# Optimization experiments

Hardware: AMD Instinct MI355X
Metric: run time of the kernel (lower is better)

Reference implementation:

```python
import jax, jax.numpy as jnp
import numpy as np

STATIC_SEQ_DIM = 48  # STAT_DIM(27) + X_TIME_DIM(13) + 8
HIDDEN = 128


def setup_inputs() -> dict:
    key = jax.random.key(0)
    ks = jax.random.split(key, 8)
    B, T = 4096, 512

    def n(k, shape, scale):
        return jax.random.normal(k, shape, dtype=jnp.float32) * scale

    return {
        "y_flow": jax.random.normal(ks[0], (B, T, 1), dtype=jnp.float32),
        "x_statics": jax.random.normal(ks[1], (B, T, STATIC_SEQ_DIM), dtype=jnp.float32),
        "twin_idx": 256,
        "enc_w1": n(ks[2], (STATIC_SEQ_DIM, STATIC_SEQ_DIM), 0.1),
        "enc_b1": jnp.zeros((STATIC_SEQ_DIM,), jnp.float32),
        "enc_w2": n(ks[3], (STATIC_SEQ_DIM, STATIC_SEQ_DIM), 0.1),
        "enc_b2": jnp.zeros((STATIC_SEQ_DIM,), jnp.float32),
        "w_ih": n(ks[4], (4 * HIDDEN, 1 + STATIC_SEQ_DIM), 0.05),
        "w_hh": n(ks[5], (4 * HIDDEN, HIDDEN), 0.05),
        "b_ih": jnp.zeros((4 * HIDDEN,), jnp.float32),
        "b_hh": jnp.zeros((4 * HIDDEN,), jnp.float32),
        "out_w": n(ks[6], (1, HIDDEN), 0.05),
        "out_b": jnp.zeros((1,), jnp.float32),
    }


def reference(y_flow, x_statics, enc_w1, enc_b1, enc_w2, enc_b2,
              w_ih, w_hh, b_ih, b_hh, out_w, out_b, twin_idx):
    B, T, _ = y_flow.shape
    H = w_hh.shape[1]
    # Static encoder MLP has no cross-time dependency -> vectorize over (B, T-1)
    xs = x_statics[:, : T - 1]                                        # (B,T-1,S)
    enc = jax.nn.relu(xs @ enc_w1.T + enc_b1) @ enc_w2.T + enc_b2     # (B,T-1,S)
    enc_t = jnp.swapaxes(enc, 0, 1)                                   # (T-1,B,S)
    flow_t = jnp.swapaxes(y_flow[:, : T - 1], 0, 1)                   # (T-1,B,1)
    ts = jnp.arange(T - 1)

    def step(carry, x):
        h, c, last_pred = carry
        flow_teacher, e_t, t = x
        flow = jnp.where(t < twin_idx - 1, flow_teacher, last_pred)   # (B,1)
        x_in = jnp.concatenate([flow, e_t], axis=-1)                  # (B,1+S)
        gates = x_in @ w_ih.T + b_ih + h @ w_hh.T + b_hh              # (B,4H)
        i, f, g, o = jnp.split(gates, 4, axis=-1)                     # torch gate order
        c_new = jax.nn.sigmoid(f) * c + jax.nn.sigmoid(i) * jnp.tanh(g)
        h_new = jax.nn.sigmoid(o) * jnp.tanh(c_new)
        pred = h_new @ out_w.T + out_b                                # (B,1)
        return (h_new, c_new, pred), pred

    h0 = jnp.zeros((B, H), jnp.float32)
    c0 = jnp.zeros((B, H), jnp.float32)
    p0 = jnp.zeros((B, 1), jnp.float32)
    _, preds = jax.lax.scan(step, (h0, c0, p0), (flow_t, enc_t, ts))  # (T-1,B,1)
    return jnp.swapaxes(preds, 0, 1)                                  # (B,T-1,1)
```

## Files before the change

### kernel.cpp

```cpp
#include <hip/hip_runtime.h>
#include <hip/hip_bf16.h>

#define HID 128
#define SDIM 48
#define NSTEP 511
#define TFULL 512
#define ROWS 16
#define XHS 200
#define HSTR 136
#define O1S 88
#define WENC_OFF 98304
#define BIAS_BYTE_OFF 208896
#define ENC_BYTE_OFF 211200
#define ENC_BYTES (4096ULL*TFULL*SDIM*2ULL)

typedef unsigned short u16;
typedef unsigned int   u32;
typedef __attribute__((ext_vector_type(8))) short short8;
typedef __attribute__((ext_vector_type(4))) float f32x4;

__device__ __forceinline__ float frcp(float x)  { return __builtin_amdgcn_rcpf(x); }
__device__ __forceinline__ float sigm(float x)  { return frcp(1.0f + __expf(-x)); }
__device__ __forceinline__ float tanh_f(float x){ return 1.0f - 2.0f*frcp(1.0f + __expf(2.0f*x)); }
__device__ __forceinline__ u16 f2bf(float f) {
  __hip_bfloat16 h = __float2bfloat16(f);
  return *reinterpret_cast<u16*>(&h);
}
__device__ __forceinline__ u32 pk2(float a, float b) {
  return (u32)f2bf(a) | ((u32)f2bf(b) << 16);
}
__device__ __forceinline__ short8 pack8(float4 a, float4 b) {
  short8 r;
  r[0]=(short)f2bf(a.x); r[1]=(short)f2bf(a.y); r[2]=(short)f2bf(a.z); r[3]=(short)f2bf(a.w);
  r[4]=(short)f2bf(b.x); r[5]=(short)f2bf(b.y); r[6]=(short)f2bf(b.z); r[7]=(short)f2bf(b.w);
  return r;
}

__global__ void setup_weights(const float* __restrict__ w_ih, const float* __restrict__ w_hh,
                              const float* __restrict__ b_ih, const float* __restrict__ b_hh,
                              const float* __restrict__ enc_w1, const float* __restrict__ enc_w2,
                              u16* __restrict__ frags, float* __restrict__ bias, int hfirst) {
  int stride = gridDim.x * blockDim.x;
  int i0 = blockIdx.x * blockDim.x + threadIdx.x;
  for (int idx = i0; idx < 32*6*64*8; idx += stride) {
    int j  = idx & 7;
    int l  = (idx >> 3) & 63;
    int kt = (idx >> 9) % 6;
    int mt = (idx >> 9) / 6;
    int gr = mt*16 + (l & 15);
    int k  = kt*32 + (l >> 4)*8 + j;
    float v = 0.f;
    if (hfirst) {
      if (k < HID)       v = w_hh[gr*HID + k];
      else if (k < 176)  v = w_ih[gr*49 + 1 + (k - HID)];
    } else {
      if (k < 48)        v = w_ih[gr*49 + 1 + k];
      else if (k < 176)  v = w_hh[gr*HID + (k - 48)];
    }
    frags[idx] = f2bf(v);
  }
  for (int idx = i0; idx < 2*3*2*64*8; idx += stride) {
    int j   = idx & 7;
    int l   = (idx >> 3) & 63;
    int kt  = (idx >> 9) & 1;
    int mt  = (idx >> 10) % 3;
    int lyr = (idx >> 10) / 3;
    int row = mt*16 + (l & 15);
    int k   = kt*32 + (l >> 4)*8 + j;
    float v = 0.f;
    if (k < SDIM) v = (lyr ? enc_w2 : enc_w1)[row*SDIM + k];
    frags[WENC_OFF + idx] = f2bf(v);
  }
  for (int idx = i0; idx < 512; idx += stride)
    bias[idx] = b_ih[idx] + b_hh[idx];
}

__global__ __launch_bounds__(256)
void enc_pre(const float* __restrict__ x_statics,
             const float* __restrict__ enc_b1, const float* __restrict__ enc_b2,
             const u16* __restrict__ frags, u16* __restrict__ enc_buf) {
  __shared__ __attribute__((aligned(16))) u16 s_o1[4][ROWS][O1S];
  const int tid = threadIdx.x;
  const int w  = tid >> 6;
  const int l  = tid & 63;
  const int lr = l & 15;
  const int lg = l >> 4;
  const int b     = blockIdx.x >> 3;
  const int chunk = blockIdx.x & 7;
  const int t = chunk*64 + w*16 + lr;

  short8 we1[3][2], we2[3][2];
  f32x4 a[3], e[3];
  #pragma unroll
  for (int mt = 0; mt < 3; ++mt) {
    #pragma unroll
    for (int kt = 0; kt < 2; ++kt) {
      we1[mt][kt] = *(const short8*)(frags + WENC_OFF + (((0*3 + mt)*2 + kt)*64 + l)*8);
      we2[mt][kt] = *(const short8*)(frags + WENC_OFF + (((1*3 + mt)*2 + kt)*64 + l)*8);
    }
    a[mt] = *(const f32x4*)&enc_b1[mt*16 + lg*4];
    e[mt] = *(const f32x4*)&enc_b2[mt*16 + lg*4];
  }

  *(unsigned long long*)&s_o1[w][l & 15][48 + (l >> 4)*4] = 0ULL;

  const float* xbase = x_statics + ((size_t)b*TFULL + t)*SDIM;
  float4 zf4 = make_float4(0.f,0.f,0.f,0.f);
  float4 c0a = *(const float4*)(xbase + lg*8);
  float4 c0b = *(const float4*)(xbase + lg*8 + 4);
  float4 c1a = zf4, c1b = zf4;
  if (lg < 2) {
    c1a = *(const float4*)(xbase + 32 + lg*8);
    c1b = *(const float4*)(xbase + 32 + lg*8 + 4);
  }
  short8 bx0 = pack8(c0a, c0b);
  short8 bx1 = pack8(c1a, c1b);

  #pragma unroll
  for (int mt = 0; mt < 3; ++mt) {
    a[mt] = __builtin_amdgcn_mfma_f32_16x16x32_bf16(we1[mt][0], bx0, a[mt], 0, 0, 0);
    a[mt] = __builtin_amdgcn_mfma_f32_16x16x32_bf16(we1[mt][1], bx1, a[mt], 0, 0, 0);
  }
  #pragma unroll
  for (int mt = 0; mt < 3; ++mt) {
    u32 lo = pk2(fmaxf(a[mt][0],0.f), fmaxf(a[mt][1],0.f));
    u32 hi = pk2(fmaxf(a[mt][2],0.f), fmaxf(a[mt][3],0.f));
    *(uint2*)&s_o1[w][lr][mt*16 + lg*4] = make_uint2(lo, hi);
  }
  asm volatile("s_waitcnt lgkmcnt(0)" ::: "memory");
  __builtin_amdgcn_sched_barrier(0);
  short8 bo0 = *(const short8*)&s_o1[w][lr][lg*8];
  short8 bo1 = *(const short8*)&s_o1[w][lr][32 + lg*8];
  #pragma unroll
  for (int mt = 0; mt < 3; ++mt) {
    e[mt] = __builtin_amdgcn_mfma_f32_16x16x32_bf16(we2[mt][0], bo0, e[mt], 0, 0, 0);
    e[mt] = __builtin_amdgcn_mfma_f32_16x16x32_bf16(we2[mt][1], bo1, e[mt], 0, 0, 0);
  }
  if (t < NSTEP) {
    u16* dst = enc_buf + ((size_t)b*TFULL + t)*SDIM;
    #pragma unroll
    for (int mt = 0; mt < 3; ++mt)
      *(uint2*)(dst + mt*16 + lg*4) = make_uint2(pk2(e[mt][0], e[mt][1]), pk2(e[mt][2], e[mt][3]));
  }
}

__global__ __launch_bounds__(512, 2)
void lstm_pre(const float* __restrict__ y_flow,
              const int* __restrict__ twin_p,
              const float* __restrict__ out_w, const float* __restrict__ out_b,
              const float* __restrict__ w_ih,
              const u16* __restrict__ frags, const float* __restrict__ bias,
              const u16* __restrict__ enc_buf,
              float* __restrict__ out) {
  __shared__ __attribute__((aligned(16))) u16   s_h[2][ROWS][HSTR];
  __shared__ __attribute__((aligned(16))) float s_pp[2][8][ROWS];

  const int tid = threadIdx.x;
  const int blk = blockIdx.x;
  const int w  = tid >> 6;
  const int l  = tid & 63;
  const int lr = l & 15;
  const int lg = l >> 4;
  const size_t b0 = (size_t)blk * ROWS;

  short8 wf[4][6];
  #pragma unroll
  for (int q = 0; q < 4; ++q)
    #pragma unroll
    for (int kt = 0; kt < 6; ++kt)
      wf[q][kt] = *(const short8*)(frags + (((w + 8*q)*6 + kt)*64 + l)*8);

  float wfl[4][4];
  #pragma unroll
  for (int q = 0; q < 4; ++q)
    #pragma unroll
    for (int r = 0; r < 4; ++r)
      wfl[q][r] = w_ih[((w + 8*q)*16 + lg*4 + r)*49];

  f32x4 bgv[4];
  #pragma unroll
  for (int q = 0; q < 4; ++q)
    bgv[q] = *(const f32x4*)&bias[(w + 8*q)*16 + lg*4];

  float owv[4];
  #pragma unroll
  for (int r = 0; r < 4; ++r) owv[r] = out_w[w*16 + lg*4 + r];
  const float ob  = out_b[0];
  const int   twc = twin_p[0] - 1;

  const u16*   erow = enc_buf + (size_t)(b0 + lr)*TFULL*SDIM;
  const float* yrow = y_flow  + (size_t)(b0 + lr)*TFULL;

  short8 encA = *(const short8*)(erow + lg*8);
  short8 encB = {};
  if (lg < 2) encB = *(const short8*)(erow + 32 + lg*8);

  for (int i = tid; i < 2*ROWS*HSTR; i += 512) ((u16*)s_h)[i] = 0;
  for (int i = tid; i < 2*8*ROWS;   i += 512) ((float*)s_pp)[i] = 0.f;
  float c_reg[4] = {0.f, 0.f, 0.f, 0.f};
  __syncthreads();

  for (int st = 0; st < NSTEP; ++st) {
    const int p  = st & 1;
    const int p2 = p ^ 1;

    short8 bh[6];
    #pragma unroll
    for (int kt = 0; kt < 4; ++kt)
      bh[kt] = *(const short8*)&s_h[p][lr][kt*32 + lg*8];
    bh[4] = encA;
    bh[5] = encB;

    float tf = 0.f;
    if (st < twc) tf = yrow[st];

    const int tt = (st + 1 < NSTEP) ? (st + 1) : (NSTEP - 1);
    encA = *(const short8*)(erow + (size_t)tt*SDIM + lg*8);
    encB = (short8){};
    if (lg < 2) encB = *(const short8*)(erow + (size_t)tt*SDIM + 32 + lg*8);

    f32x4 acc[4];
    #pragma unroll
    for (int q = 0; q < 4; ++q) acc[q] = bgv[q];
    #pragma unroll
    for (int kt = 0; kt < 6; ++kt)
      #pragma unroll
      for (int q = 0; q < 4; ++q)
        acc[q] = __builtin_amdgcn_mfma_f32_16x16x32_bf16(wf[q][kt], bh[kt], acc[q], 0, 0, 0);

    float pp01 = s_pp[p][0][lr] + s_pp[p][1][lr];
    float pp23 = s_pp[p][2][lr] + s_pp[p][3][lr];
    float pp45 = s_pp[p][4][lr] + s_pp[p][5][lr];
    float pp67 = s_pp[p][6][lr] + s_pp[p][7][lr];
    float pred_prev = ((pp01 + pp23) + (pp45 + pp67)) + ob;
    if (st == 0) pred_prev = 0.f;
    if (st > 0 && l < 16 && (l >> 1) == w)
      out[(b0 + l)*NSTEP + (st - 1)] = pred_prev;

    const float flow = (st < twc) ? tf : pred_prev;

    float hv[4];
    float hsum = 0.f;
    #pragma unroll
    for (int r = 0; r < 4; ++r) {
      float g_i = acc[0][r] + wfl[0][r]*flow;
      float g_f = acc[1][r] + wfl[1][r]*flow;
      float g_g = acc[2][r] + wfl[2][r]*flow;
      float g_o = acc[3][r] + wfl[3][r]*flow;
      float iv = sigm(g_i);
      float fv = sigm(g_f);
      float gv = tanh_f(g_g);
      float ov = sigm(g_o);
      float c  = fv*c_reg[r] + iv*gv;
      c_reg[r] = c;
      hv[r] = ov*tanh_f(c);
      hsum += hv[r]*owv[r];
    }
    *(uint2*)&s_h[p2][lr][w*16 + lg*4] = make_uint2(pk2(hv[0], hv[1]), pk2(hv[2], hv[3]));
    hsum += __shfl_xor(hsum, 16);
    hsum += __shfl_xor(hsum, 32);
    if (l < 16) s_pp[p2][w][l] = hsum;
    __syncthreads();
  }

  const int pe = NSTEP & 1;
  float pp01 = s_pp[pe][0][lr] + s_pp[pe][1][lr];
  float pp23 = s_pp[pe][2][lr] + s_pp[pe][3][lr];
  float pp45 = s_pp[pe][4][lr] + s_pp[pe][5][lr];
  float pp67 = s_pp[pe][6][lr] + s_pp[pe][7][lr];
  if (l < 16 && (l >> 1) == w)
    out[(b0 + l)*NSTEP + (NSTEP - 1)] = ((pp01 + pp23) + (pp45 + pp67)) + ob;
}

__global__ __launch_bounds__(512, 2)
void lstm_fb(const float* __restrict__ y_flow,
             const float* __restrict__ x_statics,
             const int* __restrict__ twin_p,
             const float* __restrict__ enc_b1, const float* __restrict__ enc_b2,
             const float* __restrict__ out_w, const float* __restrict__ out_b,
             const float* __restrict__ w_ih,
             const u16* __restrict__ frags, const float* __restrict__ bias,
             float* __restrict__ out) {
  __shared__ __attribute__((aligned(16))) u16   s_xh[2][ROWS][XHS];
  __shared__ __attribute__((aligned(16))) u16   s_o1[ROWS][O1S];
  __shared__ __attribute__((aligned(16))) float s_pp[2][ROWS][8];
  __shared__ __attribute__((aligned(16))) float s_bias[512];
  __shared__ __attribute__((aligned(16))) float s_eb1[SDIM];
  __shared__ __attribute__((aligned(16))) float s_eb2[SDIM];

  const int tid = threadIdx.x;
  const int blk = blockIdx.x;
  const int w  = tid >> 6;
  const int l  = tid & 63;
  const int lr = l & 15;
  const int lg = l >> 4;
  const size_t b0 = (size_t)blk * ROWS;

  short8 wf[4][6];
  #pragma unroll
  for (int q = 0; q < 4; ++q)
    #pragma unroll
    for (int kt = 0; kt < 6; ++kt)
      wf[q][kt] = *(const short8*)(frags + (((w + 8*q)*6 + kt)*64 + l)*8);

  float wfl[4][4];
  #pragma unroll
  for (int q = 0; q < 4; ++q)
    #pragma unroll
    for (int r = 0; r < 4; ++r)
      wfl[q][r] = w_ih[((w + 8*q)*16 + lg*4 + r)*49];

  short8 we1[3][2], we2[3][2];
  if (w == 7) {
    #pragma unroll
    for (int mt = 0; mt < 3; ++mt)
      #pragma unroll
      for (int kt = 0; kt < 2; ++kt) {
        we1[mt][kt] = *(const short8*)(frags + WENC_OFF + (((0*3 + mt)*2 + kt)*64 + l)*8);
        we2[mt][kt] = *(const short8*)(frags + WENC_OFF + (((1*3 + mt)*2 + kt)*64 + l)*8);
      }
  }

  float owv[4];
  #pragma unroll
  for (int r = 0; r < 4; ++r) owv[r] = out_w[w*16 + lg*4 + r];
  const float ob  = out_b[0];
  const int   twc = twin_p[0] - 1;

  for (int i = tid; i < 2*ROWS*XHS; i += 512) ((u16*)s_xh)[i] = 0;
  for (int i = tid; i < ROWS*O1S;  i += 512) ((u16*)s_o1)[i] = 0;
  for (int i = tid; i < 2*ROWS*8;  i += 512) ((float*)s_pp)[i] = 0.f;
  s_bias[tid] = bias[tid];
  if (tid < SDIM) { s_eb1[tid] = enc_b1[tid]; s_eb2[tid] = enc_b2[tid]; }
  __syncthreads();

  const float* xrow = x_statics + (size_t)(b0 + lr)*TFULL*SDIM;
  const float* yrow = y_flow    + (size_t)(b0 + lr)*TFULL;

  auto enc_step = [&](short8 bx0, short8 bx1, int pp) {
    f32x4 a[3];
    #pragma unroll
    for (int mt = 0; mt < 3; ++mt) a[mt] = *(const f32x4*)&s_eb1[mt*16 + lg*4];
    #pragma unroll
    for (int mt = 0; mt < 3; ++mt) {
      a[mt] = __builtin_amdgcn_mfma_f32_16x16x32_bf16(we1[mt][0], bx0, a[mt], 0, 0, 0);
      a[mt] = __builtin_amdgcn_mfma_f32_16x16x32_bf16(we1[mt][1], bx1, a[mt], 0, 0, 0);
    }
    #pragma unroll
    for (int mt = 0; mt < 3; ++mt) {
      *(u32*)&s_o1[lr][mt*16 + lg*4]     = pk2(fmaxf(a[mt][0],0.f), fmaxf(a[mt][1],0.f));
      *(u32*)&s_o1[lr][mt*16 + lg*4 + 2] = pk2(fmaxf(a[mt][2],0.f), fmaxf(a[mt][3],0.f));
    }
    asm volatile("s_waitcnt lgkmcnt(0)" ::: "memory");
    __builtin_amdgcn_sched_barrier(0);
    short8 bo0 = *(const short8*)&s_o1[lr][lg*8];
    short8 bo1 = *(const short8*)&s_o1[lr][32 + lg*8];
    f32x4 e[3];
    #pragma unroll
    for (int mt = 0; mt < 3; ++mt) e[mt] = *(const f32x4*)&s_eb2[mt*16 + lg*4];
    #pragma unroll
    for (int mt = 0; mt < 3; ++mt) {
      e[mt] = __builtin_amdgcn_mfma_f32_16x16x32_bf16(we2[mt][0], bo0, e[mt], 0, 0, 0);
      e[mt] = __builtin_amdgcn_mfma_f32_16x16x32_bf16(we2[mt][1], bo1, e[mt], 0, 0, 0);
    }
    #pragma unroll
    for (int mt = 0; mt < 3; ++mt) {
      *(u32*)&s_xh[pp][lr][mt*16 + lg*4]     = pk2(e[mt][0], e[mt][1]);
      *(u32*)&s_xh[pp][lr][mt*16 + lg*4 + 2] = pk2(e[mt][2], e[mt][3]);
    }
  };
  auto load_xs = [&](int t, float4& a0, float4& b0_, float4& a1, float4& b1_) {
    a0 = *(const float4*)(xrow + (size_t)t*SDIM + lg*8);
    b0_= *(const float4*)(xrow + (size_t)t*SDIM + lg*8 + 4);
    if (lg < 2) {
      a1 = *(const float4*)(xrow + (size_t)t*SDIM + 32 + lg*8);
      b1_= *(const float4*)(xrow + (size_t)t*SDIM + 32 + lg*8 + 4);
    }
  };

  float4 zf4 = make_float4(0.f, 0.f, 0.f, 0.f);
  float4 xn0a = zf4, xn0b = zf4, xn1a = zf4, xn1b = zf4;
  if (w == 7) {
    float4 c0a = zf4, c0b = zf4, c1a = zf4, c1b = zf4;
    load_xs(0, c0a, c0b, c1a, c1b);
    enc_step(pack8(c0a, c0b), pack8(c1a, c1b), 0);
    load_xs(1, xn0a, xn0b, xn1a, xn1b);
  }
  float c_reg[4] = {0.f, 0.f, 0.f, 0.f};
  __syncthreads();

  for (int st = 0; st < NSTEP; ++st) {
    const int p  = st & 1;
    const int p2 = p ^ 1;

    short8 bh[6];
    #pragma unroll
    for (int kt = 0; kt < 6; ++kt)
      bh[kt] = *(const short8*)&s_xh[p][lr][kt*32 + lg*8];

    f32x4 acc[4];
    #pragma unroll
    for (int q = 0; q < 4; ++q) acc[q] = *(const f32x4*)&s_bias[(w + 8*q)*16 + lg*4];
    #pragma unroll
    for (int kt = 0; kt < 6; ++kt)
      #pragma unroll
      for (int q = 0; q < 4; ++q)
        acc[q] = __builtin_amdgcn_mfma_f32_16x16x32_bf16(wf[q][kt], bh[kt], acc[q], 0, 0, 0);

    f32x4 pa = *(const f32x4*)&s_pp[p][lr][0];
    f32x4 pb = *(const f32x4*)&s_pp[p][lr][4];
    float pp_s = ((pa[0]+pa[1]) + (pa[2]+pa[3])) + ((pb[0]+pb[1]) + (pb[2]+pb[3]));
    float pred_prev = pp_s + ob;
    if (st == 0) pred_prev = 0.f;
    if (st > 0 && l < 16 && (l >> 1) == w)
      out[(b0 + l)*NSTEP + (st - 1)] = pred_prev;

    float tf = 0.f;
    if (st < twc) tf = yrow[st];
    const float flow = (st < twc) ? tf : pred_prev;

    if (w == 7) {
      short8 bx0 = pack8(xn0a, xn0b);
      short8 bx1 = pack8(xn1a, xn1b);
      const int tt = (st + 2 < TFULL) ? (st + 2) : (TFULL - 1);
      load_xs(tt, xn0a, xn0b, xn1a, xn1b);
      __builtin_amdgcn_s_setprio(1);
      enc_step(bx0, bx1, p2);
      __builtin_amdgcn_s_setprio(0);
    }

    float hv[4];
    float hsum = 0.f;
    #pragma unroll
    for (int r = 0; r < 4; ++r) {
      float g_i = acc[0][r] + wfl[0][r]*flow;
      float g_f = acc[1][r] + wfl[1][r]*flow;
      float g_g = acc[2][r] + wfl[2][r]*flow;
      float g_o = acc[3][r] + wfl[3][r]*flow;
      float iv = sigm(g_i);
      float fv = sigm(g_f);
      float gv = tanh_f(g_g);
      float ov = sigm(g_o);
      float c  = fv*c_reg[r] + iv*gv;
      c_reg[r] = c;
      hv[r] = ov*tanh_f(c);
      hsum += hv[r]*owv[r];
    }
    *(u32*)&s_xh[p2][lr][48 + w*16 + lg*4]     = pk2(hv[0], hv[1]);
    *(u32*)&s_xh[p2][lr][48 + w*16 + lg*4 + 2] = pk2(hv[2], hv[3]);
    hsum += __shfl_xor(hsum, 16);
    hsum += __shfl_xor(hsum, 32);
    if (l < 16) s_pp[p2][l][w] = hsum;
    __syncthreads();
  }

  f32x4 pa = *(const f32x4*)&s_pp[NSTEP & 1][lr][0];
  f32x4 pb = *(const f32x4*)&s_pp[NSTEP & 1][lr][4];
  float pp_s = ((pa[0]+pa[1]) + (pa[2]+pa[3])) + ((pb[0]+pb[1]) + (pb[2]+pb[3]));
  if (l < 16 && (l >> 1) == w)
    out[(b0 + l)*NSTEP + (NSTEP - 1)] = pp_s + ob;
}

extern "C" void kernel_launch(void* const* d_in, const int* in_sizes, int n_in,
                              void* d_out, int out_size, void* d_ws, size_t ws_size,
                              hipStream_t stream) {
  const float* y_flow    = (const float*)d_in[0];
  const float* x_statics = (const float*)d_in[1];
  const int*   twin      = (const int*)  d_in[2];
  const float* enc_w1    = (const float*)d_in[3];
  const float* enc_b1    = (const float*)d_in[4];
  const float* enc_w2    = (const float*)d_in[5];
  const float* enc_b2    = (const float*)d_in[6];
  const float* w_ih      = (const float*)d_in[7];
  const float* w_hh      = (const float*)d_in[8];
  const float* b_ih      = (const float*)d_in[9];
  const float* b_hh      = (const float*)d_in[10];
  const float* out_w     = (const float*)d_in[11];
  const float* out_b     = (const float*)d_in[12];
  float* out = (float*)d_out;

  char* ws = (char*)d_ws;
  u16*   frags   = (u16*)ws;
  float* bias    = (float*)(ws + BIAS_BYTE_OFF);
  u16*   enc_buf = (u16*)(ws + ENC_BYTE_OFF);

  const int pre = (ws_size >= (size_t)ENC_BYTE_OFF + ENC_BYTES) ? 1 : 0;

  setup_weights<<<128, 256, 0, stream>>>(w_ih, w_hh, b_ih, b_hh, enc_w1, enc_w2,
                                         frags, bias, pre);
  if (pre) {
    enc_pre<<<4096*8, 256, 0, stream>>>(x_statics, enc_b1, enc_b2, frags, enc_buf);
    lstm_pre<<<256, 512, 0, stream>>>(y_flow, twin, out_w, out_b, w_ih,
                                      frags, bias, enc_buf, out);
  } else {
    lstm_fb<<<256, 512, 0, stream>>>(y_flow, x_statics, twin,
                                     enc_b1, enc_b2, out_w, out_b, w_ih,
                                     frags, bias, out);
  }
}
```

Baseline: 901.3 us.

## Split LSTM recurrent matmul K-dimension across two wave groups

Replaces the 512-thread LSTM kernel with a 1024-thread version in which two halves of the waves each compute half of the K reduction (hidden part vs. hidden tail plus encoder features). Partial sums pass through shared memory and are combined by the second half, which also applies the gate nonlinearities. The flow input and the bias are folded into the MFMA by placing the flow value and a constant one in padding K slots, with the matching weights packed into the fragments. This halves the per-wave MFMA chain on the serial critical path, at the cost of an extra barrier per step, more LDS traffic, and bf16 rounding of the flow and bias.

```diff
diff --git a/kernel.cpp b/kernel.cpp
--- a/kernel.cpp
+++ b/kernel.cpp
@@ -8,6 +8,7 @@
 #define ROWS 16
 #define XHS 200
 #define HSTR 136
+#define PSTR 520
 #define O1S 88
 #define WENC_OFF 98304
 #define BIAS_BYTE_OFF 208896
@@ -51,11 +52,13 @@
     int k  = kt*32 + (l >> 4)*8 + j;
     float v = 0.f;
     if (hfirst) {
-      if (k < HID)       v = w_hh[gr*HID + k];
-      else if (k < 176)  v = w_ih[gr*49 + 1 + (k - HID)];
+      if (k < HID)        v = w_hh[gr*HID + k];
+      else if (k < 176)   v = w_ih[gr*49 + 1 + (k - HID)];
+      else if (k == 176)  v = w_ih[gr*49 + 0];
+      else if (k == 177)  v = b_ih[gr] + b_hh[gr];
     } else {
-      if (k < 48)        v = w_ih[gr*49 + 1 + k];
-      else if (k < 176)  v = w_hh[gr*HID + (k - 48)];
+      if (k < 48)         v = w_ih[gr*49 + 1 + k];
+      else if (k < 176)   v = w_hh[gr*HID + (k - 48)];
     }
     frags[idx] = f2bf(v);
   }
@@ -144,59 +147,51 @@
   }
 }
 
-__global__ __launch_bounds__(512, 2)
-void lstm_pre(const float* __restrict__ y_flow,
-              const int* __restrict__ twin_p,
-              const float* __restrict__ out_w, const float* __restrict__ out_b,
-              const float* __restrict__ w_ih,
-              const u16* __restrict__ frags, const float* __restrict__ bias,
-              const u16* __restrict__ enc_buf,
-              float* __restrict__ out) {
+__global__ __launch_bounds__(1024, 4)
+void lstm_ks(const float* __restrict__ y_flow,
+             const int* __restrict__ twin_p,
+             const float* __restrict__ out_w, const float* __restrict__ out_b,
+             const u16* __restrict__ frags,
+             const u16* __restrict__ enc_buf,
+             float* __restrict__ out) {
   __shared__ __attribute__((aligned(16))) u16   s_h[2][ROWS][HSTR];
+  __shared__ __attribute__((aligned(16))) float s_ps[ROWS][PSTR];
   __shared__ __attribute__((aligned(16))) float s_pp[2][8][ROWS];
 
   const int tid = threadIdx.x;
   const int blk = blockIdx.x;
-  const int w  = tid >> 6;
-  const int l  = tid & 63;
-  const int lr = l & 15;
-  const int lg = l >> 4;
+  const int w   = tid >> 6;
+  const int v   = w & 7;
+  const int sh  = w >> 3;
+  const int l   = tid & 63;
+  const int lr  = l & 15;
+  const int lg  = l >> 4;
   const size_t b0 = (size_t)blk * ROWS;
 
-  short8 wf[4][6];
+  short8 wf[4][3];
   #pragma unroll
   for (int q = 0; q < 4; ++q)
     #pragma unroll
-    for (int kt = 0; kt < 6; ++kt)
-      wf[q][kt] = *(const short8*)(frags + (((w + 8*q)*6 + kt)*64 + l)*8);
-
-  float wfl[4][4];
-  #pragma unroll
-  for (int q = 0; q < 4; ++q)
-    #pragma unroll
-    for (int r = 0; r < 4; ++r)
-      wfl[q][r] = w_ih[((w + 8*q)*16 + lg*4 + r)*49];
-
-  f32x4 bgv[4];
-  #pragma unroll
-  for (int q = 0; q < 4; ++q)
-    bgv[q] = *(const f32x4*)&bias[(w + 8*q)*16 + lg*4];
+    for (int k3 = 0; k3 < 3; ++k3)
+      wf[q][k3] = *(const short8*)(frags + (((v + 8*q)*6 + 3*sh + k3)*64 + l)*8);
 
   float owv[4];
   #pragma unroll
-  for (int r = 0; r < 4; ++r) owv[r] = out_w[w*16 + lg*4 + r];
+  for (int r = 0; r < 4; ++r) owv[r] = out_w[v*16 + lg*4 + r];
   const float ob  = out_b[0];
   const int   twc = twin_p[0] - 1;
 
   const u16*   erow = enc_buf + (size_t)(b0 + lr)*TFULL*SDIM;
   const float* yrow = y_flow  + (size_t)(b0 + lr)*TFULL;
 
-  short8 encA = *(const short8*)(erow + lg*8);
-  short8 encB = {};
-  if (lg < 2) encB = *(const short8*)(erow + 32 + lg*8);
-
-  for (int i = tid; i < 2*ROWS*HSTR; i += 512) ((u16*)s_h)[i] = 0;
-  for (int i = tid; i < 2*8*ROWS;   i += 512) ((float*)s_pp)[i] = 0.f;
+  short8 encA = {}, encB = {};
+  if (sh == 1) {
+    encA = *(const short8*)(erow + lg*8);
+    if (lg < 2) encB = *(const short8*)(erow + 32 + lg*8);
+  }
+
+  for (int i = tid; i < 2*ROWS*HSTR; i += 1024) ((u16*)s_h)[i] = 0;
+  for (int i = tid; i < 2*8*ROWS;   i += 1024) ((float*)s_pp)[i] = 0.f;
   float c_reg[4] = {0.f, 0.f, 0.f, 0.f};
   __syncthreads();
 
@@ -204,72 +199,89 @@
     const int p  = st & 1;
     const int p2 = p ^ 1;
 
-    short8 bh[6];
-    #pragma unroll
-    for (int kt = 0; kt < 4; ++kt)
-      bh[kt] = *(const short8*)&s_h[p][lr][kt*32 + lg*8];
-    bh[4] = encA;
-    bh[5] = encB;
-
-    float tf = 0.f;
-    if (st < twc) tf = yrow[st];
-
-    const int tt = (st + 1 < NSTEP) ? (st + 1) : (NSTEP - 1);
-    encA = *(const short8*)(erow + (size_t)tt*SDIM + lg*8);
-    encB = (short8){};
-    if (lg < 2) encB = *(const short8*)(erow + (size_t)tt*SDIM + 32 + lg*8);
+    short8 bh[3];
+    if (sh == 0) {
+      bh[0] = *(const short8*)&s_h[p][lr][ 0 + lg*8];
+      bh[1] = *(const short8*)&s_h[p][lr][32 + lg*8];
+      bh[2] = *(const short8*)&s_h[p][lr][64 + lg*8];
+    } else {
+      bh[0] = *(const short8*)&s_h[p][lr][96 + lg*8];
+      float pp01 = s_pp[p][0][lr] + s_pp[p][1][lr];
+      float pp23 = s_pp[p][2][lr] + s_pp[p][3][lr];
+      float pp45 = s_pp[p][4][lr] + s_pp[p][5][lr];
+      float pp67 = s_pp[p][6][lr] + s_pp[p][7][lr];
+      float pred_prev = ((pp01 + pp23) + (pp45 + pp67)) + ob;
+      if (st == 0) pred_prev = 0.f;
+      if (st > 0 && l < 16 && (l >> 1) == v)
+        out[(b0 + l)*NSTEP + (st - 1)] = pred_prev;
+      float tf = 0.f;
+      if (st < twc) tf = yrow[st];
+      const float flow = (st < twc) ? tf : pred_prev;
+      bh[1] = encA;
+      short8 b2 = encB;
+      if (lg == 2) {
+        b2[0] = (short)f2bf(flow);
+        b2[1] = (short)0x3F80;
+      }
+      bh[2] = b2;
+      const int tt = (st + 1 < NSTEP) ? (st + 1) : (NSTEP - 1);
+      encA = *(const short8*)(erow + (size_t)tt*SDIM + lg*8);
+      encB = (short8){};
+      if (lg < 2) encB = *(const short8*)(erow + (size_t)tt*SDIM + 32 + lg*8);
+    }
 
     f32x4 acc[4];
     #pragma unroll
-    for (int q = 0; q < 4; ++q) acc[q] = bgv[q];
-    #pragma unroll
-    for (int kt = 0; kt < 6; ++kt)
+    for (int q = 0; q < 4; ++q) acc[q] = (f32x4){0.f, 0.f, 0.f, 0.f};
+    #pragma unroll
+    for (int k3 = 0; k3 < 3; ++k3)
       #pragma unroll
       for (int q = 0; q < 4; ++q)
-        acc[q] = __builtin_amdgcn_mfma_f32_16x16x32_bf16(wf[q][kt], bh[kt], acc[q], 0, 0, 0);
-
-    float pp01 = s_pp[p][0][lr] + s_pp[p][1][lr];
-    float pp23 = s_pp[p][2][lr] + s_pp[p][3][lr];
-    float pp45 = s_pp[p][4][lr] + s_pp[p][5][lr];
-    float pp67 = s_pp[p][6][lr] + s_pp[p][7][lr];
-    float pred_prev = ((pp01 + pp23) + (pp45 + pp67)) + ob;
-    if (st == 0) pred_prev = 0.f;
-    if (st > 0 && l < 16 && (l >> 1) == w)
-      out[(b0 + l)*NSTEP + (st - 1)] = pred_prev;
-
-    const float flow = (st < twc) ? tf : pred_prev;
-
-    float hv[4];
-    float hsum = 0.f;
-    #pragma unroll
-    for (int r = 0; r < 4; ++r) {
-      float g_i = acc[0][r] + wfl[0][r]*flow;
-      float g_f = acc[1][r] + wfl[1][r]*flow;
-      float g_g = acc[2][r] + wfl[2][r]*flow;
-      float g_o = acc[3][r] + wfl[3][r]*flow;
-      float iv = sigm(g_i);
-      float fv = sigm(g_f);
-      float gv = tanh_f(g_g);
-      float ov = sigm(g_o);
-      float c  = fv*c_reg[r] + iv*gv;
-      c_reg[r] = c;
-      hv[r] = ov*tanh_f(c);
-      hsum += hv[r]*owv[r];
-    }
-    *(uint2*)&s_h[p2][lr][w*16 + lg*4] = make_uint2(pk2(hv[0], hv[1]), pk2(hv[2], hv[3]));
-    hsum += __shfl_xor(hsum, 16);
-    hsum += __shfl_xor(hsum, 32);
-    if (l < 16) s_pp[p2][w][l] = hsum;
+        acc[q] = __builtin_amdgcn_mfma_f32_16x16x32_bf16(wf[q][k3], bh[k3], acc[q], 0, 0, 0);
+
+    if (sh == 0) {
+      #pragma unroll
+      for (int q = 0; q < 4; ++q)
+        *(f32x4*)&s_ps[lr][(v + 8*q)*16 + lg*4] = acc[q];
+    }
     __syncthreads();
-  }
-
-  const int pe = NSTEP & 1;
-  float pp01 = s_pp[pe][0][lr] + s_pp[pe][1][lr];
-  float pp23 = s_pp[pe][2][lr] + s_pp[pe][3][lr];
-  float pp45 = s_pp[pe][4][lr] + s_pp[pe][5][lr];
-  float pp67 = s_pp[pe][6][lr] + s_pp[pe][7][lr];
-  if (l < 16 && (l >> 1) == w)
-    out[(b0 + l)*NSTEP + (NSTEP - 1)] = ((pp01 + pp23) + (pp45 + pp67)) + ob;
+
+    if (sh == 1) {
+      #pragma unroll
+      for (int q = 0; q < 4; ++q) {
+        f32x4 ps = *(const f32x4*)&s_ps[lr][(v + 8*q)*16 + lg*4];
+        acc[q] += ps;
+      }
+      float hv[4];
+      float hsum = 0.f;
+      #pragma unroll
+      for (int r = 0; r < 4; ++r) {
+        float iv = sigm(acc[0][r]);
+        float fv = sigm(acc[1][r]);
+        float gv = tanh_f(acc[2][r]);
+        float ov = sigm(acc[3][r]);
+        float c  = fv*c_reg[r] + iv*gv;
+        c_reg[r] = c;
+        hv[r] = ov*tanh_f(c);
+        hsum += hv[r]*owv[r];
+      }
+      *(uint2*)&s_h[p2][lr][v*16 + lg*4] = make_uint2(pk2(hv[0], hv[1]), pk2(hv[2], hv[3]));
+      hsum += __shfl_xor(hsum, 16);
+      hsum += __shfl_xor(hsum, 32);
+      if (l < 16) s_pp[p2][v][l] = hsum;
+    }
+    __syncthreads();
+  }
+
+  if (sh == 1) {
+    const int pe = NSTEP & 1;
+    float pp01 = s_pp[pe][0][lr] + s_pp[pe][1][lr];
+    float pp23 = s_pp[pe][2][lr] + s_pp[pe][3][lr];
+    float pp45 = s_pp[pe][4][lr] + s_pp[pe][5][lr];
+    float pp67 = s_pp[pe][6][lr] + s_pp[pe][7][lr];
+    if (l < 16 && (l >> 1) == v)
+      out[(b0 + l)*NSTEP + (NSTEP - 1)] = ((pp01 + pp23) + (pp45 + pp67)) + ob;
+  }
 }
 
 __global__ __launch_bounds__(512, 2)
@@ -490,8 +502,8 @@
                                          frags, bias, pre);
   if (pre) {
     enc_pre<<<4096*8, 256, 0, stream>>>(x_statics, enc_b1, enc_b2, frags, enc_buf);
-    lstm_pre<<<256, 512, 0, stream>>>(y_flow, twin, out_w, out_b, w_ih,
-                                      frags, bias, enc_buf, out);
+    lstm_ks<<<256, 1024, 0, stream>>>(y_flow, twin, out_w, out_b,
+                                      frags, enc_buf, out);
   } else {
     lstm_fb<<<256, 512, 0, stream>>>(y_flow, x_statics, twin,
                                      enc_b1, enc_b2, out_w, out_b, w_ih,
```

Measured after the change: 1.142 ms. +26.8%, slower.

## Fold flow input and bias into MFMA via augmented K columns with duplicated rows

Applied to the files above, without the earlier changes.

Packs the flow input weight column and the combined gate bias into spare K slots of the weight fragments, and feeds flow and a constant 1.0 through the B operand. Each step now runs two MFMA sets over duplicated 8-row halves so each lane can get its own row's flow injected, then selects the matching half. This removes per-lane scalar weight and bias registers and the VALU fused adds. In exchange it doubles the MFMA count on the serial recurrence and rounds flow to bf16.

```diff
diff --git a/kernel.cpp b/kernel.cpp
--- a/kernel.cpp
+++ b/kernel.cpp
@@ -51,11 +51,13 @@
     int k  = kt*32 + (l >> 4)*8 + j;
     float v = 0.f;
     if (hfirst) {
-      if (k < HID)       v = w_hh[gr*HID + k];
-      else if (k < 176)  v = w_ih[gr*49 + 1 + (k - HID)];
+      if (k < HID)        v = w_hh[gr*HID + k];
+      else if (k < 176)   v = w_ih[gr*49 + 1 + (k - HID)];
+      else if (k == 176)  v = w_ih[gr*49 + 0];
+      else if (k == 177)  v = b_ih[gr] + b_hh[gr];
     } else {
-      if (k < 48)        v = w_ih[gr*49 + 1 + k];
-      else if (k < 176)  v = w_hh[gr*HID + (k - 48)];
+      if (k < 48)         v = w_ih[gr*49 + 1 + k];
+      else if (k < 176)   v = w_hh[gr*HID + (k - 48)];
     }
     frags[idx] = f2bf(v);
   }
@@ -145,13 +147,12 @@
 }
 
 __global__ __launch_bounds__(512, 2)
-void lstm_pre(const float* __restrict__ y_flow,
-              const int* __restrict__ twin_p,
-              const float* __restrict__ out_w, const float* __restrict__ out_b,
-              const float* __restrict__ w_ih,
-              const u16* __restrict__ frags, const float* __restrict__ bias,
-              const u16* __restrict__ enc_buf,
-              float* __restrict__ out) {
+void lstm_dual(const float* __restrict__ y_flow,
+               const int* __restrict__ twin_p,
+               const float* __restrict__ out_w, const float* __restrict__ out_b,
+               const u16* __restrict__ frags,
+               const u16* __restrict__ enc_buf,
+               float* __restrict__ out) {
   __shared__ __attribute__((aligned(16))) u16   s_h[2][ROWS][HSTR];
   __shared__ __attribute__((aligned(16))) float s_pp[2][8][ROWS];
 
@@ -161,6 +162,7 @@
   const int l  = tid & 63;
   const int lr = l & 15;
   const int lg = l >> 4;
+  const int rA = lr & 7;
   const size_t b0 = (size_t)blk * ROWS;
 
   short8 wf[4][6];
@@ -169,18 +171,6 @@
     #pragma unroll
     for (int kt = 0; kt < 6; ++kt)
       wf[q][kt] = *(const short8*)(frags + (((w + 8*q)*6 + kt)*64 + l)*8);
-
-  float wfl[4][4];
-  #pragma unroll
-  for (int q = 0; q < 4; ++q)
-    #pragma unroll
-    for (int r = 0; r < 4; ++r)
-      wfl[q][r] = w_ih[((w + 8*q)*16 + lg*4 + r)*49];
-
-  f32x4 bgv[4];
-  #pragma unroll
-  for (int q = 0; q < 4; ++q)
-    bgv[q] = *(const f32x4*)&bias[(w + 8*q)*16 + lg*4];
 
   float owv[4];
   #pragma unroll
@@ -188,12 +178,18 @@
   const float ob  = out_b[0];
   const int   twc = twin_p[0] - 1;
 
-  const u16*   erow = enc_buf + (size_t)(b0 + lr)*TFULL*SDIM;
-  const float* yrow = y_flow  + (size_t)(b0 + lr)*TFULL;
-
-  short8 encA = *(const short8*)(erow + lg*8);
-  short8 encB = {};
-  if (lg < 2) encB = *(const short8*)(erow + 32 + lg*8);
+  const u16*   erowA = enc_buf + (size_t)(b0 + rA)*TFULL*SDIM;
+  const u16*   erowB = enc_buf + (size_t)(b0 + 8 + rA)*TFULL*SDIM;
+  const float* yrowA = y_flow  + (size_t)(b0 + rA)*TFULL;
+  const float* yrowB = y_flow  + (size_t)(b0 + 8 + rA)*TFULL;
+
+  short8 eA0 = *(const short8*)(erowA + lg*8);
+  short8 eA1 = *(const short8*)(erowB + lg*8);
+  short8 eB0 = {}, eB1 = {};
+  if (lg < 2) {
+    eB0 = *(const short8*)(erowA + 32 + lg*8);
+    eB1 = *(const short8*)(erowB + 32 + lg*8);
+  }
 
   for (int i = tid; i < 2*ROWS*HSTR; i += 512) ((u16*)s_h)[i] = 0;
   for (int i = tid; i < 2*8*ROWS;   i += 512) ((float*)s_pp)[i] = 0.f;
@@ -204,53 +200,73 @@
     const int p  = st & 1;
     const int p2 = p ^ 1;
 
-    short8 bh[6];
-    #pragma unroll
-    for (int kt = 0; kt < 4; ++kt)
-      bh[kt] = *(const short8*)&s_h[p][lr][kt*32 + lg*8];
-    bh[4] = encA;
-    bh[5] = encB;
-
-    float tf = 0.f;
-    if (st < twc) tf = yrow[st];
+    float tfA = 0.f, tfB = 0.f;
+    if (st < twc) { tfA = yrowA[st]; tfB = yrowB[st]; }
+
+    short8 bhA[6], bhB[6];
+    #pragma unroll
+    for (int kt = 0; kt < 4; ++kt) {
+      bhA[kt] = *(const short8*)&s_h[p][rA][kt*32 + lg*8];
+      bhB[kt] = *(const short8*)&s_h[p][8 + rA][kt*32 + lg*8];
+    }
+    bhA[4] = eA0;
+    bhB[4] = eA1;
+
+    float pA = 0.f, pB = 0.f;
+    #pragma unroll
+    for (int ww = 0; ww < 8; ++ww) {
+      pA += s_pp[p][ww][rA];
+      pB += s_pp[p][ww][8 + rA];
+    }
+    float predA = pA + ob, predB = pB + ob;
+    if (st == 0) { predA = 0.f; predB = 0.f; }
+    if (st > 0 && l < 16 && (l >> 1) == w)
+      out[(b0 + l)*NSTEP + (st - 1)] = (l < 8) ? predA : predB;
+
+    const float flowA = (st < twc) ? tfA : predA;
+    const float flowB = (st < twc) ? tfB : predB;
+
+    short8 b5A = eB0, b5B = eB1;
+    if (lg == 2) {
+      b5A[0] = (short)f2bf(flowA); b5A[1] = (short)0x3F80;
+      b5B[0] = (short)f2bf(flowB); b5B[1] = (short)0x3F80;
+    }
+    bhA[5] = b5A;
+    bhB[5] = b5B;
 
     const int tt = (st + 1 < NSTEP) ? (st + 1) : (NSTEP - 1);
-    encA = *(const short8*)(erow + (size_t)tt*SDIM + lg*8);
-    encB = (short8){};
-    if (lg < 2) encB = *(const short8*)(erow + (size_t)tt*SDIM + 32 + lg*8);
-
-    f32x4 acc[4];
-    #pragma unroll
-    for (int q = 0; q < 4; ++q) acc[q] = bgv[q];
+    eA0 = *(const short8*)(erowA + (size_t)tt*SDIM + lg*8);
+    eA1 = *(const short8*)(erowB + (size_t)tt*SDIM + lg*8);
+    eB0 = (short8){}; eB1 = (short8){};
+    if (lg < 2) {
+      eB0 = *(const short8*)(erowA + (size_t)tt*SDIM + 32 + lg*8);
+      eB1 = *(const short8*)(erowB + (size_t)tt*SDIM + 32 + lg*8);
+    }
+
+    f32x4 aA[4], aB[4];
+    #pragma unroll
+    for (int q = 0; q < 4; ++q) { aA[q] = (f32x4){0,0,0,0}; aB[q] = (f32x4){0,0,0,0}; }
     #pragma unroll
     for (int kt = 0; kt < 6; ++kt)
       #pragma unroll
-      for (int q = 0; q < 4; ++q)
-        acc[q] = __builtin_amdgcn_mfma_f32_16x16x32_bf16(wf[q][kt], bh[kt], acc[q], 0, 0, 0);
-
-    float pp01 = s_pp[p][0][lr] + s_pp[p][1][lr];
-    float pp23 = s_pp[p][2][lr] + s_pp[p][3][lr];
-    float pp45 = s_pp[p][4][lr] + s_pp[p][5][lr];
-    float pp67 = s_pp[p][6][lr] + s_pp[p][7][lr];
-    float pred_prev = ((pp01 + pp23) + (pp45 + pp67)) + ob;
-    if (st == 0) pred_prev = 0.f;
-    if (st > 0 && l < 16 && (l >> 1) == w)
-      out[(b0 + l)*NSTEP + (st - 1)] = pred_prev;
-
-    const float flow = (st < twc) ? tf : pred_prev;
+      for (int q = 0; q < 4; ++q) {
+        aA[q] = __builtin_amdgcn_mfma_f32_16x16x32_bf16(wf[q][kt], bhA[kt], aA[q], 0, 0, 0);
+        aB[q] = __builtin_amdgcn_mfma_f32_16x16x32_bf16(wf[q][kt], bhB[kt], aB[q], 0, 0, 0);
+      }
+
+    const bool isA = (lr < 8);
+    f32x4 G[4];
+    #pragma unroll
+    for (int q = 0; q < 4; ++q) G[q] = isA ? aA[q] : aB[q];
 
     float hv[4];
     float hsum = 0.f;
     #pragma unroll
     for (int r = 0; r < 4; ++r) {
-      float g_i = acc[0][r] + wfl[0][r]*flow;
-      float g_f = acc[1][r] + wfl[1][r]*flow;
-      float g_g = acc[2][r] + wfl[2][r]*flow;
-      float g_o = acc[3][r] + wfl[3][r]*flow;
-      float iv = sigm(g_i);
-      float fv = sigm(g_f);
-      float gv = tanh_f(g_g);
-      float ov = sigm(g_o);
+      float iv = sigm(G[0][r]);
+      float fv = sigm(G[1][r]);
+      float gv = tanh_f(G[2][r]);
+      float ov = sigm(G[3][r]);
       float c  = fv*c_reg[r] + iv*gv;
       c_reg[r] = c;
       hv[r] = ov*tanh_f(c);
@@ -264,12 +280,14 @@
   }
 
   const int pe = NSTEP & 1;
-  float pp01 = s_pp[pe][0][lr] + s_pp[pe][1][lr];
-  float pp23 = s_pp[pe][2][lr] + s_pp[pe][3][lr];
-  float pp45 = s_pp[pe][4][lr] + s_pp[pe][5][lr];
-  float pp67 = s_pp[pe][6][lr] + s_pp[pe][7][lr];
+  float pA = 0.f, pB = 0.f;
+  #pragma unroll
+  for (int ww = 0; ww < 8; ++ww) {
+    pA += s_pp[pe][ww][rA];
+    pB += s_pp[pe][ww][8 + rA];
+  }
   if (l < 16 && (l >> 1) == w)
-    out[(b0 + l)*NSTEP + (NSTEP - 1)] = ((pp01 + pp23) + (pp45 + pp67)) + ob;
+    out[(b0 + l)*NSTEP + (NSTEP - 1)] = ((l < 8) ? pA : pB) + ob;
 }
 
 __global__ __launch_bounds__(512, 2)
@@ -490,8 +508,8 @@
                                          frags, bias, pre);
   if (pre) {
     enc_pre<<<4096*8, 256, 0, stream>>>(x_statics, enc_b1, enc_b2, frags, enc_buf);
-    lstm_pre<<<256, 512, 0, stream>>>(y_flow, twin, out_w, out_b, w_ih,
-                                      frags, bias, enc_buf, out);
+    lstm_dual<<<256, 512, 0, stream>>>(y_flow, twin, out_w, out_b,
+                                       frags, enc_buf, out);
   } else {
     lstm_fb<<<256, 512, 0, stream>>>(y_flow, x_statics, twin,
                                      enc_b1, enc_b2, out_w, out_b, w_ih,
```

Result: slower. 1.167 ms (+29.4%).
